# Kernel tuning notes

Measured on AMD Instinct MI355X. Metric: run time of the kernel, lower is better.

The kernel has to match this reference:

```python
import jax, jax.numpy as jnp
import numpy as np

K = 20
BN_EPS = 1e-5
NEG_SLOPE = 0.2


def knn_idx(x, k):
    # x: [B, C, N]; returns indices of k nearest neighbors per point: [B, N, k]
    sq = jnp.sum(x * x, axis=1)                      # [B, N]
    inner = jnp.einsum('bcn,bcm->bnm', x, x)         # [B, N, N]
    dist = sq[:, :, None] + sq[:, None, :] - 2.0 * inner  # squared distances
    _, idx = jax.lax.top_k(-dist, k)                 # smallest distances
    return idx


def get_graph_feature(x, k):
    # x: [B, C, N] -> [B, 2C, N, k]
    idx = knn_idx(x, k)                               # [B, N, k]
    gather = lambda xb, ib: xb[:, ib]                 # [C,N] x [N,k] -> [C,N,k]
    feature = jax.vmap(gather)(x, idx)                # [B, C, N, k]
    xk = jnp.broadcast_to(x[:, :, :, None], feature.shape)
    return jnp.concatenate([feature - xk, xk], axis=1)  # [B, 2C, N, k]


def setup_inputs() -> dict:
    key = jax.random.key(0)
    k1, k2 = jax.random.split(key)
    B, C, N = 8, 64, 4096
    x = jax.random.normal(k1, (B, C, N), dtype=jnp.float32)
    W = jax.random.normal(k2, (64, 2 * C), dtype=jnp.float32) * (1.0 / np.sqrt(2 * C))
    gamma = jnp.ones((64,), dtype=jnp.float32)
    beta = jnp.zeros((64,), dtype=jnp.float32)
    return {"x": x, "W": W, "gamma": gamma, "beta": beta}


def reference(x, W, gamma, beta):
    g = get_graph_feature(x, K)                       # [B, 2C, N, k]
    y = jnp.einsum('oc,bcnk->bonk', W, g)             # 1x1 conv, no bias
    # BatchNorm2d (training-mode batch statistics) over (B, N, k) per channel
    mean = jnp.mean(y, axis=(0, 2, 3), keepdims=True)
    var = jnp.var(y, axis=(0, 2, 3), keepdims=True)
    y = (y - mean) * jax.lax.rsqrt(var + BN_EPS)
    y = y * gamma[None, :, None, None] + beta[None, :, None, None]
    # LeakyReLU(0.2)
    y = jnp.where(y >= 0, y, NEG_SLOPE * y)
    # max over neighbors
    return jnp.max(y, axis=-1)                        # [B, out, N]
```

## Files before the change

kernel.cpp:

```cpp
#include <hip/hip_runtime.h>
#include <hip/hip_bf16.h>
#include <float.h>

#define BATCH 8
#define CDIM 64
#define NPTS 4096
#define KNN 20
#define KSEL 32
#define BUFCAP 128
#define BN_EPS 1e-5f
#define NEG_SLOPE 0.2f

typedef __attribute__((ext_vector_type(8))) short short8;
typedef __attribute__((ext_vector_type(4))) float float4v;
typedef unsigned short ushort;
typedef unsigned int uint;
typedef unsigned long long ull;

__device__ __forceinline__ ushort f2bf(float f) {
    uint u = __float_as_uint(f);
    u += 0x7FFF + ((u >> 16) & 1);
    return (ushort)(u >> 16);
}
__device__ __forceinline__ int mbcnt64(ull m) {
    int c = __builtin_amdgcn_mbcnt_lo((uint)m, 0);
    return __builtin_amdgcn_mbcnt_hi((uint)(m >> 32), c);
}

__device__ __forceinline__ uint select33_truncate(uint* __restrict__ buf,
                                                  int& cnt, int lane) {
    uint e0 = 0xFFFFFFFFu, e1 = 0xFFFFFFFFu;
    if (lane < cnt) e0 = buf[lane];
    if (64 + lane < cnt) e1 = buf[64 + lane];
    uint p = 0;
    for (int bit = 31; bit >= 0; --bit) {
        uint t = p | (1u << bit);
        ull mA = __ballot(e0 < t);
        ull mB = __ballot(e1 < t);
        if (__popcll(mA) + __popcll(mB) < 33) p = t;
    }
    ull mA = __ballot(e0 < p);
    ull mB = __ballot(e1 < p);
    int pA = __popcll(mA);
    int r0 = mbcnt64(mA);
    int r1 = pA + mbcnt64(mB);
    if (e0 < p) buf[r0] = e0;
    if (e1 < p) buf[r1] = e1;
    cnt = pA + __popcll(mB);
    return p;
}

__device__ __forceinline__ void scan_append(float dwv, float base, int idx,
                                            uint& tau, int& cnt,
                                            uint* __restrict__ buf, int lane) {
    float dval = fmaxf(fmaf(-2.f, dwv, base), 0.f);
    uint key = (__float_as_uint(dval) & 0xFFFFF000u) | (uint)idx;
    ull mask = __ballot(key < tau);
    if (mask) {
        int c = __popcll(mask);
        if (cnt + c > BUFCAP) {
            tau = select33_truncate(buf, cnt, lane);
            mask = __ballot(key < tau);
            c = __popcll(mask);
        }
        if (c) {
            int rank = mbcnt64(mask);
            if (key < tau) buf[cnt + rank] = key;
            cnt += c;
        }
    }
}

__global__ void k_prep(const float* __restrict__ x,
                       float* __restrict__ xt,
                       ushort* __restrict__ xh,
                       float* __restrict__ sq) {
    int gid = blockIdx.x * 256 + threadIdx.x;
    int b = gid >> 12;
    int n = gid & (NPTS - 1);
    const float* xb = x + (size_t)b * CDIM * NPTS + n;
    float acc = 0.f;
    float4* xtv = (float4*)(xt + ((size_t)gid << 6));
    uint2* xhp = (uint2*)(xh + ((size_t)gid << 6));
    #pragma unroll
    for (int q = 0; q < 16; ++q) {
        float v[4]; ushort h[4];
        #pragma unroll
        for (int j = 0; j < 4; ++j) {
            float tv = xb[(q * 4 + j) * NPTS];
            v[j] = tv;
            acc = fmaf(tv, tv, acc);
            h[j] = f2bf(tv);
        }
        xtv[q] = make_float4(v[0], v[1], v[2], v[3]);
        uint2 ph;
        ph.x = (uint)h[0] | ((uint)h[1] << 16);
        ph.y = (uint)h[2] | ((uint)h[3] << 16);
        xhp[q] = ph;
    }
    sq[gid] = acc;
}

__global__ void k_pz(const float* __restrict__ xt, const float* __restrict__ W,
                     float* __restrict__ pt, float* __restrict__ zt) {
    int b  = blockIdx.x >> 6;
    int n0 = (blockIdx.x & 63) << 6;
    int lane = threadIdx.x & 63;
    int w = threadIdx.x >> 6;
    int n = n0 + lane;
    size_t rowoff = ((size_t)(b * NPTS + n)) << 6;
    const float4* xrow = (const float4*)(xt + rowoff);
    float acc1[16], acc2[16];
    #pragma unroll
    for (int i = 0; i < 16; ++i) { acc1[i] = 0.f; acc2[i] = 0.f; }
    #pragma unroll
    for (int cg = 0; cg < 4; ++cg) {
        float xv[16];
        #pragma unroll
        for (int q = 0; q < 4; ++q) {
            float4 t = xrow[cg * 4 + q];
            xv[q*4] = t.x; xv[q*4+1] = t.y; xv[q*4+2] = t.z; xv[q*4+3] = t.w;
        }
        #pragma unroll
        for (int oi = 0; oi < 16; ++oi) {
            int o = (w << 4) + oi;
            const float* wr = W + o * 128 + cg * 16;
            float a1 = acc1[oi], a2 = acc2[oi];
            #pragma unroll
            for (int j = 0; j < 16; ++j) {
                a1 = fmaf(wr[j],      xv[j], a1);
                a2 = fmaf(wr[64 + j], xv[j], a2);
            }
            acc1[oi] = a1; acc2[oi] = a2;
        }
    }
    float4* pv = (float4*)(pt + rowoff + (w << 4));
    float4* zv = (float4*)(zt + rowoff + (w << 4));
    #pragma unroll
    for (int q = 0; q < 4; ++q) {
        pv[q] = make_float4(acc1[q*4], acc1[q*4+1], acc1[q*4+2], acc1[q*4+3]);
        zv[q] = make_float4(acc2[q*4]   - acc1[q*4],
                            acc2[q*4+1] - acc1[q*4+1],
                            acc2[q*4+2] - acc1[q*4+2],
                            acc2[q*4+3] - acc1[q*4+3]);
    }
}

__global__ void __launch_bounds__(256, 8) k_knn(
        const ushort* __restrict__ xh,
        const float* __restrict__ sq, ushort* __restrict__ knn32) {
    __shared__ float dw[2][16][68];
    __shared__ uint rowbuf[16 * BUFCAP];

    int tid  = threadIdx.x;
    int t    = tid >> 6;
    int lane = tid & 63;
    int b    = blockIdx.x >> 8;
    int r0   = (blockIdx.x & 255) << 4;
    int col  = lane & 15;
    int quad = lane >> 4;

    size_t arow = ((size_t)(b * NPTS + r0 + col)) << 6;
    short8 ah0 = *(const short8*)(xh + arow + quad * 8);
    short8 ah1 = *(const short8*)(xh + arow + 32 + quad * 8);

    const ushort* xhb = xh + (((size_t)b * NPTS) << 6);
    const float* sqb = sq + b * NPTS;
    const ushort* fbase = xhb + (((size_t)((t << 4) + col)) << 6) + (quad << 3);

    uint tau[4];
    int cnt[4];
    float sqr[4];
    uint* wbuf = rowbuf + ((t << 2) * BUFCAP);
    #pragma unroll
    for (int r = 0; r < 4; ++r) {
        tau[r] = 0xFFFFFFFFu; cnt[r] = 0;
        sqr[r] = sqb[r0 + (t << 2) + r];
    }

    short8 fA0 = *(const short8*)fbase;
    short8 fA1 = *(const short8*)(fbase + 32);
    short8 fB0, fB1;
    float sv_cur = 0.f;
    float sv_nxt = sqb[lane];

    auto step = [&](int c, int q, short8& f0, short8& f1,
                    short8& nf0, short8& nf1) {
        if (c + 1 < 64) {
            const ushort* p = fbase + (((size_t)(c + 1)) << 12);
            nf0 = *(const short8*)p;
            nf1 = *(const short8*)(p + 32);
        }
        float sv_tmp = (c + 1 < 64) ? sqb[((c + 1) << 6) + lane] : 0.f;

        float4v acc = {0.f, 0.f, 0.f, 0.f};
        acc = __builtin_amdgcn_mfma_f32_16x16x32_bf16(ah0, f0, acc, 0, 0, 0);
        acc = __builtin_amdgcn_mfma_f32_16x16x32_bf16(ah1, f1, acc, 0, 0, 0);
        #pragma unroll
        for (int r = 0; r < 4; ++r)
            dw[q][(quad << 2) + r][(t << 4) + col] = acc[r];

        if (c > 0) {
            int m0 = (c - 1) << 6;
            #pragma unroll
            for (int r = 0; r < 4; ++r) {
                float dv = dw[q ^ 1][(t << 2) + r][lane];
                scan_append(dv, sv_cur + sqr[r], m0 + lane, tau[r], cnt[r],
                            wbuf + r * BUFCAP, lane);
            }
        }
        sv_cur = sv_nxt;
        sv_nxt = sv_tmp;

        __builtin_amdgcn_sched_barrier(0);
        asm volatile("s_waitcnt lgkmcnt(0)" ::: "memory");
        __builtin_amdgcn_s_barrier();
        __builtin_amdgcn_sched_barrier(0);
    };

    for (int c = 0; c < 64; c += 2) {
        step(c,     0, fA0, fA1, fB0, fB1);
        step(c + 1, 1, fB0, fB1, fA0, fA1);
    }

    {
        int m0 = 63 << 6;
        #pragma unroll
        for (int r = 0; r < 4; ++r) {
            float dv = dw[1][(t << 2) + r][lane];
            scan_append(dv, sv_cur + sqr[r], m0 + lane, tau[r], cnt[r],
                        wbuf + r * BUFCAP, lane);
        }
    }

    #pragma unroll
    for (int r = 0; r < 4; ++r) {
        select33_truncate(wbuf + r * BUFCAP, cnt[r], lane);
        if (lane < KSEL) {
            uint e = wbuf[r * BUFCAP + lane];
            knn32[(size_t)(b * NPTS + r0 + (t << 2) + r) * KSEL + lane] =
                (ushort)(e & 0xFFFu);
        }
    }
}

__global__ void __launch_bounds__(256) k_refine(
        const float* __restrict__ xt, const float* __restrict__ sq,
        const ushort* __restrict__ knn32, int* __restrict__ idx20) {
    int wvid = (blockIdx.x << 2) + (threadIdx.x >> 6);
    int lane = threadIdx.x & 63;
    int half = lane >> 5;
    int sl   = lane & 31;
    int row  = (wvid << 1) + half;
    int b = row >> 12;
    int cand = knn32[(size_t)row * KSEL + sl];
    const float4* xc = (const float4*)(xt + ((size_t)(b * NPTS + cand) << 6));
    const float4* xr = (const float4*)(xt + ((size_t)row << 6));
    float acc = 0.f;
    #pragma unroll
    for (int q = 0; q < 16; ++q) {
        float4 a = xr[q], c = xc[q];
        acc = fmaf(a.x, c.x, acc); acc = fmaf(a.y, c.y, acc);
        acc = fmaf(a.z, c.z, acc); acc = fmaf(a.w, c.w, acc);
    }
    float d = fmaf(-2.f, acc, sq[b * NPTS + cand]);
    int rank = 0;
    int base = half << 5;
    #pragma unroll
    for (int j = 0; j < KSEL; ++j) {
        float dj = __shfl(d, base + j);
        int   cj = __shfl(cand, base + j);
        rank += ((dj < d) || (dj == d && cj < cand)) ? 1 : 0;
    }
    if (rank < KNN)
        idx20[(size_t)row * KNN + rank] = cand;
}

__global__ void k_gather(const float* __restrict__ pt, const float* __restrict__ zt,
                         const int* __restrict__ idxin,
                         float* __restrict__ tmax, float* __restrict__ tmin,
                         float* __restrict__ S1, float* __restrict__ S2) {
    __shared__ float red1[4][64];
    __shared__ float red2[4][64];
    int b  = blockIdx.x >> 6;
    int n0 = (blockIdx.x & 63) << 6;
    int lane = threadIdx.x & 63;
    int w = threadIdx.x >> 6;
    float cs1 = 0.f, cs2 = 0.f;
    for (int i = 0; i < 16; ++i) {
        int n = n0 + (w << 4) + i;
        int base = b * NPTS + n;
        int ibase = __builtin_amdgcn_readfirstlane(base * KNN);
        const int* ip = idxin + ibase;
        float mx = -FLT_MAX, mn = FLT_MAX, s1 = 0.f, s2 = 0.f;
        #pragma unroll
        for (int k = 0; k < KNN; ++k) {
            int colp = ip[k];
            float v = pt[(((size_t)(b * NPTS + colp)) << 6) + lane];
            mx = fmaxf(mx, v); mn = fminf(mn, v);
            s1 += v; s2 = fmaf(v, v, s2);
        }
        float z = zt[(((size_t)base) << 6) + lane];
        tmax[(((size_t)base) << 6) + lane] = mx + z;
        tmin[(((size_t)base) << 6) + lane] = mn + z;
        cs1 += s1 + (float)KNN * z;
        cs2 += s2 + 2.f * z * s1 + (float)KNN * z * z;
    }
    red1[w][lane] = cs1;
    red2[w][lane] = cs2;
    __syncthreads();
    if (threadIdx.x < 64) {
        float t1 = red1[0][lane] + red1[1][lane] + red1[2][lane] + red1[3][lane];
        float t2 = red2[0][lane] + red2[1][lane] + red2[2][lane] + red2[3][lane];
        atomicAdd(&S1[lane], t1);
        atomicAdd(&S2[lane], t2);
    }
}

__global__ void k_final(const float* __restrict__ tmax, const float* __restrict__ tmin,
                        const float* __restrict__ S1, const float* __restrict__ S2,
                        const float* __restrict__ gamma, const float* __restrict__ beta,
                        float* __restrict__ out) {
    __shared__ float smx[64][65];
    __shared__ float smn[64][65];
    int b  = blockIdx.x >> 6;
    int n0 = (blockIdx.x & 63) << 6;
    int lane = threadIdx.x & 63;
    int w = threadIdx.x >> 6;
    #pragma unroll
    for (int i = 0; i < 16; ++i) {
        int nl = (i << 2) + w;
        size_t off = (((size_t)(b * NPTS + n0 + nl)) << 6) + lane;
        smx[nl][lane] = tmax[off];
        smn[nl][lane] = tmin[off];
    }
    __syncthreads();
    const float inv_cnt = 1.0f / ((float)BATCH * NPTS * KNN);
    #pragma unroll
    for (int i = 0; i < 16; ++i) {
        int o = (i << 2) + w;
        float s1 = S1[o], s2 = S2[o];
        float mean = s1 * inv_cnt;
        float var = fmaf(-mean, mean, s2 * inv_cnt);
        float rs = rsqrtf(var + BN_EPS);
        float sc = gamma[o] * rs;
        float sh = beta[o] - mean * sc;
        float tv = (sc >= 0.f) ? smx[lane][o] : smn[lane][o];
        float y = fmaf(tv, sc, sh);
        y = (y >= 0.f) ? y : NEG_SLOPE * y;
        out[((size_t)(b * 64 + o)) * NPTS + n0 + lane] = y;
    }
}

extern "C" void kernel_launch(void* const* d_in, const int* in_sizes, int n_in,
                              void* d_out, int out_size, void* d_ws, size_t ws_size,
                              hipStream_t stream) {
    const float* x     = (const float*)d_in[0];
    const float* W     = (const float*)d_in[1];
    const float* gamma = (const float*)d_in[2];
    const float* beta  = (const float*)d_in[3];
    float* out = (float*)d_out;

    float* ws = (float*)d_ws;
    const size_t SECT = (size_t)BATCH * NPTS * 64;
    float*  xt    = ws;
    float*  pt    = ws + SECT;
    float*  zt    = ws + 2 * SECT;
    float*  sq    = ws + 3 * SECT;
    float*  S1    = ws + 3 * SECT + 32768;
    float*  S2    = S1 + 64;
    int*    idx20 = (int*)(ws + 3 * SECT + 32768 + 128);
    float*  uA    = ws + 3 * SECT + 32768 + 128 + 655360;
    ushort* xh    = (ushort*)uA;
    ushort* knn32 = (ushort*)(uA + SECT / 2);
    float*  tmx   = uA;
    float*  tmn   = uA + SECT;

    hipMemsetAsync(S1, 0, 2 * 64 * sizeof(float), stream);
    k_prep  <<<dim3((BATCH * NPTS) / 256), dim3(256), 0, stream>>>(x, xt, xh, sq);
    k_pz    <<<dim3(BATCH * (NPTS / 64)), dim3(256), 0, stream>>>(xt, W, pt, zt);
    k_knn   <<<dim3(BATCH * (NPTS / 16)), dim3(256), 0, stream>>>(xh, sq, knn32);
    k_refine<<<dim3((BATCH * NPTS) / 8), dim3(256), 0, stream>>>(xt, sq, knn32, idx20);
    k_gather<<<dim3(BATCH * (NPTS / 64)), dim3(256), 0, stream>>>(pt, zt, idx20, tmx, tmn, S1, S2);
    k_final <<<dim3(BATCH * (NPTS / 64)), dim3(256), 0, stream>>>(tmx, tmn, S1, S2, gamma, beta, out);
}
```

Measured before the change: 355.5 us.

## Fuse prep and projection kernels; vectorize kNN distance tile LDS traffic

Merges the transpose/bf16-convert/square-norm kernel with the per-point W projection kernel. The transposed tile is staged in shared memory, so the projection no longer re-reads xt from global memory and one launch goes away. In the kNN kernel, the distance tile layout changes to [64][20] so each MFMA result is written as one float4 and each lane reads its four rows as one float4, replacing eight scalar LDS accesses per step. The new layout may add bank conflicts, and the fused kernel uses more shared memory per block.

```diff
diff --git a/kernel.cpp b/kernel.cpp
--- a/kernel.cpp
+++ b/kernel.cpp
@@ -71,45 +71,55 @@
     }
 }
 
-__global__ void k_prep(const float* __restrict__ x,
-                       float* __restrict__ xt,
-                       ushort* __restrict__ xh,
-                       float* __restrict__ sq) {
-    int gid = blockIdx.x * 256 + threadIdx.x;
-    int b = gid >> 12;
-    int n = gid & (NPTS - 1);
-    const float* xb = x + (size_t)b * CDIM * NPTS + n;
-    float acc = 0.f;
-    float4* xtv = (float4*)(xt + ((size_t)gid << 6));
-    uint2* xhp = (uint2*)(xh + ((size_t)gid << 6));
-    #pragma unroll
-    for (int q = 0; q < 16; ++q) {
-        float v[4]; ushort h[4];
-        #pragma unroll
-        for (int j = 0; j < 4; ++j) {
-            float tv = xb[(q * 4 + j) * NPTS];
-            v[j] = tv;
-            acc = fmaf(tv, tv, acc);
-            h[j] = f2bf(tv);
-        }
-        xtv[q] = make_float4(v[0], v[1], v[2], v[3]);
-        uint2 ph;
-        ph.x = (uint)h[0] | ((uint)h[1] << 16);
-        ph.y = (uint)h[2] | ((uint)h[3] << 16);
-        xhp[q] = ph;
-    }
-    sq[gid] = acc;
-}
-
-__global__ void k_pz(const float* __restrict__ xt, const float* __restrict__ W,
-                     float* __restrict__ pt, float* __restrict__ zt) {
+__global__ void __launch_bounds__(256) k_ppz(
+        const float* __restrict__ x, const float* __restrict__ W,
+        float* __restrict__ xt, ushort* __restrict__ xh,
+        float* __restrict__ sq,
+        float* __restrict__ pt, float* __restrict__ zt) {
+    __shared__ float xs[64][65];
+    __shared__ float sqred[4][64];
+
     int b  = blockIdx.x >> 6;
     int n0 = (blockIdx.x & 63) << 6;
     int lane = threadIdx.x & 63;
     int w = threadIdx.x >> 6;
-    int n = n0 + lane;
-    size_t rowoff = ((size_t)(b * NPTS + n)) << 6;
-    const float4* xrow = (const float4*)(xt + rowoff);
+    int row = b * NPTS + n0 + lane;
+
+    const float* xb = x + (size_t)b * CDIM * NPTS + (n0 + lane);
+    float v[16]; ushort h[16];
+    float accq = 0.f;
+    #pragma unroll
+    for (int j = 0; j < 16; ++j) {
+        float tv = xb[((w << 4) + j) * NPTS];
+        v[j] = tv;
+        accq = fmaf(tv, tv, accq);
+        h[j] = f2bf(tv);
+        xs[lane][(w << 4) + j] = tv;
+    }
+    {
+        float4* xtv = (float4*)(xt + ((size_t)row << 6) + (w << 4));
+        #pragma unroll
+        for (int q = 0; q < 4; ++q)
+            xtv[q] = make_float4(v[q*4], v[q*4+1], v[q*4+2], v[q*4+3]);
+        uint4* xhp = (uint4*)(xh + ((size_t)row << 6) + (w << 4));
+        uint4 p0, p1;
+        p0.x = (uint)h[0] | ((uint)h[1] << 16);
+        p0.y = (uint)h[2] | ((uint)h[3] << 16);
+        p0.z = (uint)h[4] | ((uint)h[5] << 16);
+        p0.w = (uint)h[6] | ((uint)h[7] << 16);
+        p1.x = (uint)h[8] | ((uint)h[9] << 16);
+        p1.y = (uint)h[10] | ((uint)h[11] << 16);
+        p1.z = (uint)h[12] | ((uint)h[13] << 16);
+        p1.w = (uint)h[14] | ((uint)h[15] << 16);
+        xhp[0] = p0; xhp[1] = p1;
+    }
+    sqred[w][lane] = accq;
+    __syncthreads();
+    if (w == 0)
+        sq[row] = sqred[0][lane] + sqred[1][lane] +
+                  sqred[2][lane] + sqred[3][lane];
+
+    size_t rowoff = ((size_t)row) << 6;
     float acc1[16], acc2[16];
     #pragma unroll
     for (int i = 0; i < 16; ++i) { acc1[i] = 0.f; acc2[i] = 0.f; }
@@ -117,10 +127,8 @@
     for (int cg = 0; cg < 4; ++cg) {
         float xv[16];
         #pragma unroll
-        for (int q = 0; q < 4; ++q) {
-            float4 t = xrow[cg * 4 + q];
-            xv[q*4] = t.x; xv[q*4+1] = t.y; xv[q*4+2] = t.z; xv[q*4+3] = t.w;
-        }
+        for (int j = 0; j < 16; ++j)
+            xv[j] = xs[lane][(cg << 4) + j];
         #pragma unroll
         for (int oi = 0; oi < 16; ++oi) {
             int o = (w << 4) + oi;
@@ -149,7 +157,7 @@
 __global__ void __launch_bounds__(256, 8) k_knn(
         const ushort* __restrict__ xh,
         const float* __restrict__ sq, ushort* __restrict__ knn32) {
-    __shared__ float dw[2][16][68];
+    __shared__ float dw[2][64][20];
     __shared__ uint rowbuf[16 * BUFCAP];
 
     int tid  = threadIdx.x;
@@ -196,16 +204,14 @@
         float4v acc = {0.f, 0.f, 0.f, 0.f};
         acc = __builtin_amdgcn_mfma_f32_16x16x32_bf16(ah0, f0, acc, 0, 0, 0);
         acc = __builtin_amdgcn_mfma_f32_16x16x32_bf16(ah1, f1, acc, 0, 0, 0);
-        #pragma unroll
-        for (int r = 0; r < 4; ++r)
-            dw[q][(quad << 2) + r][(t << 4) + col] = acc[r];
+        *(float4v*)&dw[q][(t << 4) + col][quad << 2] = acc;
 
         if (c > 0) {
             int m0 = (c - 1) << 6;
+            float4v dv4 = *(const float4v*)&dw[q ^ 1][lane][t << 2];
             #pragma unroll
             for (int r = 0; r < 4; ++r) {
-                float dv = dw[q ^ 1][(t << 2) + r][lane];
-                scan_append(dv, sv_cur + sqr[r], m0 + lane, tau[r], cnt[r],
+                scan_append(dv4[r], sv_cur + sqr[r], m0 + lane, tau[r], cnt[r],
                             wbuf + r * BUFCAP, lane);
             }
         }
@@ -225,10 +231,10 @@
 
     {
         int m0 = 63 << 6;
+        float4v dv4 = *(const float4v*)&dw[1][lane][t << 2];
         #pragma unroll
         for (int r = 0; r < 4; ++r) {
-            float dv = dw[1][(t << 2) + r][lane];
-            scan_append(dv, sv_cur + sqr[r], m0 + lane, tau[r], cnt[r],
+            scan_append(dv4[r], sv_cur + sqr[r], m0 + lane, tau[r], cnt[r],
                         wbuf + r * BUFCAP, lane);
         }
     }
@@ -377,8 +383,7 @@
     float*  tmn   = uA + SECT;
 
     hipMemsetAsync(S1, 0, 2 * 64 * sizeof(float), stream);
-    k_prep  <<<dim3((BATCH * NPTS) / 256), dim3(256), 0, stream>>>(x, xt, xh, sq);
-    k_pz    <<<dim3(BATCH * (NPTS / 64)), dim3(256), 0, stream>>>(xt, W, pt, zt);
+    k_ppz   <<<dim3(BATCH * (NPTS / 64)), dim3(256), 0, stream>>>(x, W, xt, xh, sq, pt, zt);
     k_knn   <<<dim3(BATCH * (NPTS / 16)), dim3(256), 0, stream>>>(xh, sq, knn32);
     k_refine<<<dim3((BATCH * NPTS) / 8), dim3(256), 0, stream>>>(xt, sq, knn32, idx20);
     k_gather<<<dim3(BATCH * (NPTS / 64)), dim3(256), 0, stream>>>(pt, zt, idx20, tmx, tmn, S1, S2);
```

After: 328.4 us. 1.08x faster.
